# Kernel optimization log

Measured on AMD Instinct MI355X. Metric: run time of the kernel, lower is better.

The kernel has to match this reference:

```python
import jax, jax.numpy as jnp
import numpy as np

B, NW, NS, SL = 32, 500, 50, 40
EMB, HID, VOCAB, E = 300, 150, 50000, 563200
N = B * (NW + NS)
MAXPOS = 512


def _sinusoid(n_pos, d):
    pos = np.arange(n_pos)[:, None].astype(np.float64)
    i = np.arange(d)[None, :]
    ang = pos / np.power(10000.0, 2 * (i // 2) / d)
    tab = np.zeros((n_pos, d))
    tab[:, 0::2] = np.sin(ang[:, 0::2])
    tab[:, 1::2] = np.cos(ang[:, 1::2])
    tab[0] = 0.0  # padding_idx=0
    return jnp.asarray(tab, dtype=jnp.float32)

_POS_TAB = _sinusoid(MAXPOS + 1, EMB)


def setup_inputs():
    keys = iter(jax.random.split(jax.random.key(0), 48))
    def nrm(shape, s=0.05):
        return jax.random.normal(next(keys), shape, dtype=jnp.float32) * s
    inp = {}
    inp["x"] = jax.random.randint(next(keys), (B, NW), 0, VOCAB, dtype=jnp.int32)
    inp["sent_x"] = jax.random.randint(next(keys), (B, NS, SL), 0, VOCAB, dtype=jnp.int32)
    inp["edge_index"] = jax.random.randint(next(keys), (2, E), 0, N, dtype=jnp.int32)
    inp["embed_table"] = nrm((VOCAB, EMB)).at[0].set(0.0)  # padding_idx=0
    for h in range(2, 8):
        inp["conv_w%d" % h] = nrm((50, 1, h, EMB))
        inp["conv_b%d" % h] = nrm((50,))
    inp["cnn_proj_w"] = nrm((HID, EMB)); inp["cnn_proj_b"] = nrm((HID,))
    inp["lstm_w_ih_l0"] = nrm((2, 4 * HID, HID)); inp["lstm_w_hh_l0"] = nrm((2, 4 * HID, HID))
    inp["lstm_b_ih_l0"] = nrm((2, 4 * HID)); inp["lstm_b_hh_l0"] = nrm((2, 4 * HID))
    inp["lstm_w_ih_l1"] = nrm((2, 4 * HID, 2 * HID)); inp["lstm_w_hh_l1"] = nrm((2, 4 * HID, HID))
    inp["lstm_b_ih_l1"] = nrm((2, 4 * HID)); inp["lstm_b_hh_l1"] = nrm((2, 4 * HID))
    inp["lstm_proj_w"] = nrm((HID, 2 * HID)); inp["lstm_proj_b"] = nrm((HID,))
    inp["gc0_w"] = nrm((HID, EMB)); inp["gc0_b"] = nrm((HID,))
    inp["gc1_w"] = nrm((HID, HID)); inp["gc1_b"] = nrm((HID,))
    inp["gc2_w"] = nrm((HID, HID)); inp["gc2_b"] = nrm((HID,))
    return inp


def _forward(x, sent_x, edge_index, embed_table, conv_ws, conv_bs,
             cnn_proj_w, cnn_proj_b, w_ih0, w_hh0, b_ih0, b_hh0,
             w_ih1, w_hh1, b_ih1, b_hh1, lstm_proj_w, lstm_proj_b,
             gc0_w, gc0_b, gc1_w, gc1_b, gc2_w, gc2_b):
    Bsz, S, L = sent_x.shape
    Nn = Bsz * S
    emb_words = embed_table[x]                                   # [B, NW, EMB]
    tok = embed_table[sent_x].reshape(Nn, L, EMB)                # [Nn, L, EMB]
    sentlen = (sent_x != 0).sum(-1).reshape(Nn)                  # token count per sentence
    a = jnp.arange(L)
    input_pos = jnp.where(a[None, :] < sentlen[:, None], a[None, :] + 1, 0)
    enc = tok + _POS_TAB[input_pos]
    # CNN ngram features: conv heights 2..7, full-width kernels == windowed matmuls
    feats = []
    for w, b in zip(conv_ws, conv_bs):
        h = w.shape[2]
        acc = b + sum(jnp.einsum('nld,od->nlo', enc[:, k:L - h + 1 + k, :], w[:, 0, k, :]) for k in range(h))
        feats.append(jnp.max(jax.nn.relu(acc), axis=1))          # [Nn, 50]
    ngram = jnp.concatenate(feats, axis=1)                        # [Nn, 300]
    snode_pos = jnp.tile(jnp.arange(S), Bsz)
    cnn_feat = ((ngram + _POS_TAB[snode_pos]) @ cnn_proj_w.T + cnn_proj_b).reshape(Bsz, S, HID)
    glen = (sent_x[:, :, 0] != 0).sum(-1)                         # valid sentence count per graph

    def lstm_dir(xs, w_ih, w_hh, bias):
        def step(carry, xt):
            hh, cc = carry
            g = xt @ w_ih.T + hh @ w_hh.T + bias
            i, f, gg, o = jnp.split(g, 4, axis=-1)
            cc = jax.nn.sigmoid(f) * cc + jax.nn.sigmoid(i) * jnp.tanh(gg)
            hh = jax.nn.sigmoid(o) * jnp.tanh(cc)
            return (hh, cc), hh
        z = jnp.zeros((xs.shape[0], HID), xs.dtype)
        _, hs = jax.lax.scan(step, (z, z), jnp.swapaxes(xs, 0, 1))
        return jnp.swapaxes(hs, 0, 1)

    def rev_within(xs):
        # reverse only the first glen[b] steps (packed-sequence semantics)
        T = xs.shape[1]; t = jnp.arange(T)
        idx = jnp.where(t[None, :] < glen[:, None], glen[:, None] - 1 - t[None, :], t[None, :])
        return jnp.take_along_axis(xs, idx[:, :, None], axis=1)

    def bidir(xs, w_ih, w_hh, b_i, b_h):
        f = lstm_dir(xs, w_ih[0], w_hh[0], b_i[0] + b_h[0])
        r = rev_within(lstm_dir(rev_within(xs), w_ih[1], w_hh[1], b_i[1] + b_h[1]))
        return jnp.concatenate([f, r], axis=-1)

    h1 = bidir(cnn_feat, w_ih0, w_hh0, b_ih0, b_hh0)
    h2 = bidir(h1, w_ih1, w_hh1, b_ih1, b_hh1)
    mask = (jnp.arange(S)[None, :] < glen[:, None]).astype(h2.dtype)[:, :, None]
    lstm_feat = (h2 * mask) @ lstm_proj_w.T + lstm_proj_b
    sent_out = jnp.concatenate([cnn_feat, lstm_feat], axis=-1)    # [B, S, 300]
    nodes = jnp.concatenate([emb_words, sent_out], axis=1)        # [B, NW+S, 300]
    nodes = (nodes @ gc0_w.T + gc0_b).reshape(-1, HID)            # [N, 150]
    Nt = nodes.shape[0]
    loop = jnp.arange(Nt, dtype=edge_index.dtype)
    src = jnp.concatenate([edge_index[0], loop])                  # add self-loops
    dst = jnp.concatenate([edge_index[1], loop])
    deg = jax.ops.segment_sum(jnp.ones(src.shape[0], nodes.dtype), dst, num_segments=Nt)
    dis = jnp.where(deg > 0, jax.lax.rsqrt(deg), 0.0)
    norm = (dis[src] * dis[dst])[:, None]

    def gcn(xin, w, bias):
        xw = xin @ w.T
        return jax.ops.segment_sum(xw[src] * norm, dst, num_segments=Nt) + bias

    h = jax.nn.elu(gcn(nodes, gc1_w, gc1_b))
    # F.dropout with training=False -> identity
    return gcn(h, gc2_w, gc2_b), emb_words


def reference(x, sent_x, edge_index, embed_table, conv_w2, conv_b2, conv_w3, conv_b3,
              conv_w4, conv_b4, conv_w5, conv_b5, conv_w6, conv_b6, conv_w7, conv_b7,
              cnn_proj_w, cnn_proj_b, lstm_w_ih_l0, lstm_w_hh_l0, lstm_b_ih_l0, lstm_b_hh_l0,
              lstm_w_ih_l1, lstm_w_hh_l1, lstm_b_ih_l1, lstm_b_hh_l1, lstm_proj_w, lstm_proj_b,
              gc0_w, gc0_b, gc1_w, gc1_b, gc2_w, gc2_b):
    conv_ws = [conv_w2, conv_w3, conv_w4, conv_w5, conv_w6, conv_w7]
    conv_bs = [conv_b2, conv_b3, conv_b4, conv_b5, conv_b6, conv_b7]
    return _forward(x, sent_x, edge_index, embed_table, conv_ws, conv_bs,
                    cnn_proj_w, cnn_proj_b, lstm_w_ih_l0, lstm_w_hh_l0, lstm_b_ih_l0, lstm_b_hh_l0,
                    lstm_w_ih_l1, lstm_w_hh_l1, lstm_b_ih_l1, lstm_b_hh_l1, lstm_proj_w, lstm_proj_b,
                    gc0_w, gc0_b, gc1_w, gc1_b, gc2_w, gc2_b)
```

## Files before the change

kernel.cpp:

```cpp
#include <hip/hip_runtime.h>
#include <stdint.h>
#include <math.h>

#define EDGES 563200
#define NNODES 17600
#define OUT0SZ 2640000
#define MROWS 64000
#define MPAD  64016
#define KSTRIDE 2112

typedef _Float16 h2 __attribute__((ext_vector_type(2)));
typedef _Float16 h4 __attribute__((ext_vector_type(4)));
typedef _Float16 v8h __attribute__((ext_vector_type(8)));
typedef float v4f __attribute__((ext_vector_type(4)));

__device__ __forceinline__ float sigm(float x){ return 1.f / (1.f + expf(-x)); }

__device__ __forceinline__ float fdot2_(h2 a, h2 b, float c){
#if __has_builtin(__builtin_amdgcn_fdot2)
  return __builtin_amdgcn_fdot2(a, b, c, false);
#else
  return c + (float)a.x * (float)b.x + (float)a.y * (float)b.y;
#endif
}

__device__ __forceinline__ void stage16(const char* g, char* lds_base, int lane){
#if __has_builtin(__builtin_amdgcn_global_load_lds)
  __builtin_amdgcn_global_load_lds(
      (const __attribute__((address_space(1))) void*)g,
      (__attribute__((address_space(3))) void*)lds_base, 16, 0, 0);
#else
  uint4 v = *(const uint4*)g;
  *(uint4*)(lds_base + lane * 16) = v;
#endif
}

__global__ void gcnk_postab(float* __restrict__ pos){
  int idx = blockIdx.x * 256 + threadIdx.x;
  if (idx >= 513 * 300) return;
  int p = idx / 300, i = idx - p * 300;
  float v = 0.f;
  if (p != 0){
    double expo = (double)(2 * (i / 2)) / 300.0;
    double ang = (double)p / pow(10000.0, expo);
    v = (float)((i & 1) ? cos(ang) : sin(ang));
  }
  pos[idx] = v;
}

__global__ __launch_bounds__(1024)
void gcnk_prep2(const int* __restrict__ sx, int* __restrict__ sentlen,
                int* __restrict__ glen_g, int* __restrict__ rowmap){
  __shared__ int sg[32];
  int tid = threadIdx.x;
  for (int i = tid; i < 1600; i += 1024){
    int c = 0;
    for (int j = 0; j < 40; j++) c += (sx[i * 40 + j] != 0);
    sentlen[i] = c;
  }
  if (tid < 32){
    int c = 0;
    for (int s = 0; s < 50; s++) c += (sx[tid * 2000 + s * 40] != 0);
    glen_g[tid] = c; sg[tid] = c;
  }
  __syncthreads();
  for (int i = tid; i < 1600; i += 1024){
    int b = i / 50, t = i - b * 50, g = sg[b];
    rowmap[i] = b * 50 + ((t < g) ? (g - 1 - t) : t);
  }
}

__global__ void gcnk_embw(const int* __restrict__ x, const float* __restrict__ tab,
                          float4* __restrict__ out){
  int idx = blockIdx.x * 256 + threadIdx.x;
  if (idx >= 16000 * 75) return;
  int row = idx / 75, q = idx - row * 75;
  const float4* t = (const float4*)tab;
  out[idx] = t[x[row] * 75 + q];
}

__global__ void gcnk_zeroi(unsigned int* __restrict__ p, int n){
  int i = blockIdx.x * 256 + threadIdx.x;
  if (i < n) p[i] = 0u;
}

__global__ void gcnk_ench(const int* __restrict__ sx, const float* __restrict__ tab,
                          const float* __restrict__ pos, const int* __restrict__ sentlen,
                          _Float16* __restrict__ ench){
  int idx = blockIdx.x * 256 + threadIdx.x;
  if (idx >= MPAD * 75) return;
  int row = idx / 75, q = idx - row * 75;
  int d = q * 4;
  h4 o; o[0] = (_Float16)0.f; o[1] = (_Float16)0.f; o[2] = (_Float16)0.f; o[3] = (_Float16)0.f;
  if (row < MROWS){
    int n = row / 40, l = row - n * 40;
    int tok = sx[n * 40 + l];
    int p = (l < sentlen[n]) ? (l + 1) : 0;
    float4 a = *(const float4*)(tab + (size_t)tok * 300 + d);
    float4 b = *(const float4*)(pos + (size_t)p * 300 + d);
    o[0] = (_Float16)(a.x + b.x); o[1] = (_Float16)(a.y + b.y);
    o[2] = (_Float16)(a.z + b.z); o[3] = (_Float16)(a.w + b.w);
  }
  *(h4*)(ench + (size_t)row * 300 + d) = o;
}

__global__ void gcnk_bpack(const float* w2, const float* w3, const float* w4,
                           const float* w5, const float* w6, const float* w7,
                           const float* c2, const float* c3, const float* c4,
                           const float* c5, const float* c6, const float* c7,
                           _Float16* __restrict__ Bp, float* __restrict__ bias_p){
  int idx = blockIdx.x * 256 + threadIdx.x;
  if (idx < 2 * 160 * KSTRIDE){
    int n = idx / KSTRIDE, kk = idx - n * KSTRIDE;
    int g = n / 160, c = n - g * 160;
    _Float16 v = (_Float16)0.f;
    if (c < 150){
      int H = 3 * g + 2 + c / 50, o = c % 50;
      if (kk < 300 * H){
        const float* w;
        switch (H){ case 2: w = w2; break; case 3: w = w3; break;
                    case 4: w = w4; break; case 5: w = w5; break;
                    case 6: w = w6; break; default: w = w7; break; }
        v = (_Float16)w[o * 300 * H + kk];
      }
    }
    Bp[idx] = v;
  }
  if (idx < 320){
    int g = idx / 160, c = idx - g * 160;
    float bv = 0.f;
    if (c < 150){
      int H = 3 * g + 2 + c / 50, o = c % 50;
      const float* cbp;
      switch (H){ case 2: cbp = c2; break; case 3: cbp = c3; break;
                  case 4: cbp = c4; break; case 5: cbp = c5; break;
                  case 6: cbp = c6; break; default: cbp = c7; break; }
      bv = cbp[o];
    }
    bias_p[idx] = bv;
  }
}

__global__ __launch_bounds__(256)
void gcnk_convmfma(const _Float16* __restrict__ A, const _Float16* __restrict__ Bp,
                   const float* __restrict__ bias_p, unsigned int* __restrict__ ngram_u){
  __shared__ __align__(1024) char smem[36864];
  _Float16* Asm = (_Float16*)smem;
  _Float16* Bsm = (_Float16*)(smem + 16384);
  float* Cs = (float*)smem;
  const int tid = threadIdx.x;
  const int m0 = blockIdx.x * 128;
  const int grp = blockIdx.y;
  const char* Abase = (const char*)A;
  const char* Bbase = (const char*)(Bp + (size_t)grp * 160 * KSTRIDE);
  const int kmax = grp ? 2112 : 1216;
  const int w = tid >> 6, lane = tid & 63;
  const int wm = (w >> 1) * 64, wn = (w & 1) * 80;
  const int fm = lane & 15, fq = lane >> 4;
  const int lrow = lane >> 3;
  const int loff = (((lane & 7) ^ lrow) << 4);

  v4f acc[4][5] = {};

  for (int kc = 0; kc < kmax; kc += 64){
    #pragma unroll
    for (int ii = 0; ii < 4; ii++){
      int i = w * 4 + ii;
      const char* g = Abase + (size_t)(m0 + i * 8 + lrow) * 600 + kc * 2 + loff;
      stage16(g, (char*)Asm + i * 1024, lane);
    }
    #pragma unroll
    for (int jj = 0; jj < 5; jj++){
      int j = w * 5 + jj;
      const char* g = Bbase + (size_t)(j * 8 + lrow) * (KSTRIDE * 2) + kc * 2 + loff;
      stage16(g, (char*)Bsm + j * 1024, lane);
    }
    __syncthreads();
    #pragma unroll
    for (int ks = 0; ks < 2; ks++){
      const int axor = (ks * 64 + fq * 16) ^ ((fm & 7) << 4);
      v8h af[4], bf[5];
      #pragma unroll
      for (int mt = 0; mt < 4; mt++)
        af[mt] = *(const v8h*)((const char*)Asm + (wm + mt * 16 + fm) * 128 + axor);
      #pragma unroll
      for (int nt = 0; nt < 5; nt++)
        bf[nt] = *(const v8h*)((const char*)Bsm + (wn + nt * 16 + fm) * 128 + axor);
      #pragma unroll
      for (int mt = 0; mt < 4; mt++)
        #pragma unroll
        for (int nt = 0; nt < 5; nt++)
          acc[mt][nt] = __builtin_amdgcn_mfma_f32_16x16x32_f16(af[mt], bf[nt], acc[mt][nt], 0, 0, 0);
    }
    __syncthreads();
  }

  for (int p = 0; p < 5; p++){
    __syncthreads();
    #pragma unroll
    for (int nt = 0; nt < 5; nt++){
      int cstart = wn + nt * 16;
      if ((cstart >> 5) == p){
        int co = cstart - p * 32 + fm;
        #pragma unroll
        for (int mt = 0; mt < 4; mt++)
          #pragma unroll
          for (int r = 0; r < 4; r++)
            Cs[(wm + mt * 16 + fq * 4 + r) * 33 + co] = acc[mt][nt][r];
      }
    }
    __syncthreads();
    if (tid < 128){
      int cl = tid & 31, si = tid >> 5;
      int col = p * 32 + cl;
      if (col < 150){
        int H = 3 * grp + 2 + col / 50, lh = 41 - H;
        int sent = m0 / 40 + si;
        if (sent < 1600){
          int rlo = sent * 40; if (rlo < m0) rlo = m0;
          int rhi = sent * 40 + lh; if (rhi > m0 + 128) rhi = m0 + 128;
          if (rlo < rhi){
            float bv = bias_p[grp * 160 + col];
            float vmax = 0.f;
            for (int r = rlo; r < rhi; r++){
              float v = Cs[(r - m0) * 33 + cl] + bv;
              vmax = fmaxf(vmax, v);
            }
            atomicMax(ngram_u + sent * 300 + grp * 150 + col, __float_as_uint(vmax));
          }
        }
      }
    }
  }
}

template<int BM, int BN, int WMT, int WNT, int OUTH>
__global__ __launch_bounds__(256)
void gcnk_mgemm(const float* __restrict__ A, const float* __restrict__ Wt,
                const float* __restrict__ b1, const float* __restrict__ b2,
                void* __restrict__ Cv, int M, int N, int K){
  __shared__ __align__(16) _Float16 As[BM * 40];
  __shared__ __align__(16) _Float16 Bs[BN * 40];
  const int tid = threadIdx.x;
  const int m0 = blockIdx.x * BM, n0 = blockIdx.y * BN;
  const int w = tid >> 6, lane = tid & 63;
  const int wm = (w >> 1) * (WMT * 16), wn = (w & 1) * (WNT * 16);
  const int fm = lane & 15, fq = lane >> 4;
  v4f acc[WMT][WNT] = {};
  const int nch = (K + 31) >> 5;
  for (int ch = 0; ch < nch; ch++){
    int kc = ch * 32;
    #pragma unroll
    for (int j = 0; j < BM / 64; j++){
      int u = tid + 256 * j;
      int row = u >> 2, cb = (u & 3) * 8;
      int gm = m0 + row, gk = kc + cb;
      v8h vv;
      if (gm < M && gk + 8 <= K){
        const float2* p = (const float2*)(A + (size_t)gm * K + gk);
        float2 q0 = p[0], q1 = p[1], q2 = p[2], q3 = p[3];
        vv[0] = (_Float16)q0.x; vv[1] = (_Float16)q0.y;
        vv[2] = (_Float16)q1.x; vv[3] = (_Float16)q1.y;
        vv[4] = (_Float16)q2.x; vv[5] = (_Float16)q2.y;
        vv[6] = (_Float16)q3.x; vv[7] = (_Float16)q3.y;
      } else {
        #pragma unroll
        for (int e = 0; e < 8; e++)
          vv[e] = (gm < M && gk + e < K) ? (_Float16)A[(size_t)gm * K + gk + e] : (_Float16)0.f;
      }
      *(v8h*)(As + row * 40 + cb) = vv;
    }
    {
      int row = tid >> 2, cb = (tid & 3) * 8;
      int gn = n0 + row, gk = kc + cb;
      v8h vv;
      if (gn < N && gk + 8 <= K){
        const float2* p = (const float2*)(Wt + (size_t)gn * K + gk);
        float2 q0 = p[0], q1 = p[1], q2 = p[2], q3 = p[3];
        vv[0] = (_Float16)q0.x; vv[1] = (_Float16)q0.y;
        vv[2] = (_Float16)q1.x; vv[3] = (_Float16)q1.y;
        vv[4] = (_Float16)q2.x; vv[5] = (_Float16)q2.y;
        vv[6] = (_Float16)q3.x; vv[7] = (_Float16)q3.y;
      } else {
        #pragma unroll
        for (int e = 0; e < 8; e++)
          vv[e] = (gn < N && gk + e < K) ? (_Float16)Wt[(size_t)gn * K + gk + e] : (_Float16)0.f;
      }
      *(v8h*)(Bs + row * 40 + cb) = vv;
    }
    __syncthreads();
    v8h af[WMT], bf[WNT];
    #pragma unroll
    for (int mt = 0; mt < WMT; mt++)
      af[mt] = *(const v8h*)(As + (wm + mt * 16 + fm) * 40 + fq * 8);
    #pragma unroll
    for (int nt = 0; nt < WNT; nt++)
      bf[nt] = *(const v8h*)(Bs + (wn + nt * 16 + fm) * 40 + fq * 8);
    #pragma unroll
    for (int mt = 0; mt < WMT; mt++)
      #pragma unroll
      for (int nt = 0; nt < WNT; nt++)
        acc[mt][nt] = __builtin_amdgcn_mfma_f32_16x16x32_f16(af[mt], bf[nt], acc[mt][nt], 0, 0, 0);
    __syncthreads();
  }
  #pragma unroll
  for (int nt = 0; nt < WNT; nt++){
    int gn = n0 + wn + nt * 16 + fm;
    if (gn >= N) continue;
    float badd = (b1 ? b1[gn] : 0.f) + (b2 ? b2[gn] : 0.f);
    #pragma unroll
    for (int mt = 0; mt < WMT; mt++)
      #pragma unroll
      for (int r = 0; r < 4; r++){
        int gm = m0 + wm + mt * 16 + fq * 4 + r;
        if (gm < M){
          float val = acc[mt][nt][r] + badd;
          if (OUTH) ((_Float16*)Cv)[(size_t)gm * 160 + gn] = (_Float16)val;
          else      ((float*)Cv)[(size_t)gm * N + gn] = val;
        }
      }
  }
}

__global__ __launch_bounds__(256)
void gcnk_mgemmF(const float* __restrict__ A1, const int* __restrict__ mapA,
                 const float* __restrict__ A2, const int* __restrict__ mapB,
                 const int* __restrict__ glen, int usemask,
                 const float* __restrict__ apos,
                 const float* __restrict__ Wt, const float* __restrict__ b1,
                 const float* __restrict__ b2, float* __restrict__ C,
                 int M, int N, int K){
  const int BM = 64, WMT = 2, WNT = 2;
  __shared__ __align__(16) _Float16 As[BM * 40];
  __shared__ __align__(16) _Float16 Bs[64 * 40];
  const int tid = threadIdx.x;
  const int m0 = blockIdx.x * BM, n0 = blockIdx.y * 64;
  const int w = tid >> 6, lane = tid & 63;
  const int wm = (w >> 1) * (WMT * 16), wn = (w & 1) * (WNT * 16);
  const int fm = lane & 15, fq = lane >> 4;
  v4f acc[WMT][WNT] = {};
  const int nch = (K + 31) >> 5;
  for (int ch = 0; ch < nch; ch++){
    int kc = ch * 32;
    {
      int row = tid >> 2, cb = (tid & 3) * 8;
      int gm = m0 + row, gk = kc + cb;
      v8h vv;
      bool ok = (gm < M);
      if (ok && usemask){
        int b = gm / 50;
        if (gm - b * 50 >= glen[b]) ok = false;
      }
      if (!ok){
        #pragma unroll
        for (int e = 0; e < 8; e++) vv[e] = (_Float16)0.f;
      } else if (!A2){
        int r = mapA ? mapA[gm] : gm;
        const float* base = A1 + (size_t)r * K;
        if (gk + 8 <= K){
          const float2* p = (const float2*)(base + gk);
          float2 q0 = p[0], q1 = p[1], q2 = p[2], q3 = p[3];
          if (apos){
            const float2* a2 = (const float2*)(apos + (size_t)(gm % 50) * K + gk);
            float2 r0 = a2[0], r1 = a2[1], r2 = a2[2], r3 = a2[3];
            q0.x += r0.x; q0.y += r0.y; q1.x += r1.x; q1.y += r1.y;
            q2.x += r2.x; q2.y += r2.y; q3.x += r3.x; q3.y += r3.y;
          }
          vv[0] = (_Float16)q0.x; vv[1] = (_Float16)q0.y;
          vv[2] = (_Float16)q1.x; vv[3] = (_Float16)q1.y;
          vv[4] = (_Float16)q2.x; vv[5] = (_Float16)q2.y;
          vv[6] = (_Float16)q3.x; vv[7] = (_Float16)q3.y;
        } else {
          #pragma unroll
          for (int e = 0; e < 8; e++){
            int c = gk + e;
            float vf = (c < K) ? base[c] : 0.f;
            if (apos && c < K) vf += apos[(size_t)(gm % 50) * K + c];
            vv[e] = (_Float16)vf;
          }
        }
      } else {
        int rA = mapA ? mapA[gm] : gm;
        int rB = mapB ? mapB[gm] : gm;
        const float* pa = A1 + (size_t)rA * 150;
        const float* pb = A2 + (size_t)rB * 150;
        if (gk + 8 <= 150){
          const float2* p = (const float2*)(pa + gk);
          float2 q0 = p[0], q1 = p[1], q2 = p[2], q3 = p[3];
          vv[0] = (_Float16)q0.x; vv[1] = (_Float16)q0.y;
          vv[2] = (_Float16)q1.x; vv[3] = (_Float16)q1.y;
          vv[4] = (_Float16)q2.x; vv[5] = (_Float16)q2.y;
          vv[6] = (_Float16)q3.x; vv[7] = (_Float16)q3.y;
        } else if (gk >= 152 && gk + 8 <= K){
          const float2* p = (const float2*)(pb + gk - 150);
          float2 q0 = p[0], q1 = p[1], q2 = p[2], q3 = p[3];
          vv[0] = (_Float16)q0.x; vv[1] = (_Float16)q0.y;
          vv[2] = (_Float16)q1.x; vv[3] = (_Float16)q1.y;
          vv[4] = (_Float16)q2.x; vv[5] = (_Float16)q2.y;
          vv[6] = (_Float16)q3.x; vv[7] = (_Float16)q3.y;
        } else {
          #pragma unroll
          for (int e = 0; e < 8; e++){
            int c = gk + e;
            vv[e] = (c < 150) ? (_Float16)pa[c]
                  : ((c < K) ? (_Float16)pb[c - 150] : (_Float16)0.f);
          }
        }
      }
      *(v8h*)(As + row * 40 + cb) = vv;
    }
    {
      int row = tid >> 2, cb = (tid & 3) * 8;
      int gn = n0 + row, gk = kc + cb;
      v8h vv;
      if (gn < N && gk + 8 <= K){
        const float2* p = (const float2*)(Wt + (size_t)gn * K + gk);
        float2 q0 = p[0], q1 = p[1], q2 = p[2], q3 = p[3];
        vv[0] = (_Float16)q0.x; vv[1] = (_Float16)q0.y;
        vv[2] = (_Float16)q1.x; vv[3] = (_Float16)q1.y;
        vv[4] = (_Float16)q2.x; vv[5] = (_Float16)q2.y;
        vv[6] = (_Float16)q3.x; vv[7] = (_Float16)q3.y;
      } else {
        #pragma unroll
        for (int e = 0; e < 8; e++)
          vv[e] = (gn < N && gk + e < K) ? (_Float16)Wt[(size_t)gn * K + gk + e] : (_Float16)0.f;
      }
      *(v8h*)(Bs + row * 40 + cb) = vv;
    }
    __syncthreads();
    v8h af[WMT], bf[WNT];
    #pragma unroll
    for (int mt = 0; mt < WMT; mt++)
      af[mt] = *(const v8h*)(As + (wm + mt * 16 + fm) * 40 + fq * 8);
    #pragma unroll
    for (int nt = 0; nt < WNT; nt++)
      bf[nt] = *(const v8h*)(Bs + (wn + nt * 16 + fm) * 40 + fq * 8);
    #pragma unroll
    for (int mt = 0; mt < WMT; mt++)
      #pragma unroll
      for (int nt = 0; nt < WNT; nt++)
        acc[mt][nt] = __builtin_amdgcn_mfma_f32_16x16x32_f16(af[mt], bf[nt], acc[mt][nt], 0, 0, 0);
    __syncthreads();
  }
  #pragma unroll
  for (int nt = 0; nt < WNT; nt++){
    int gn = n0 + wn + nt * 16 + fm;
    if (gn >= N) continue;
    float badd = (b1 ? b1[gn] : 0.f) + (b2 ? b2[gn] : 0.f);
    #pragma unroll
    for (int mt = 0; mt < WMT; mt++)
      #pragma unroll
      for (int r = 0; r < 4; r++){
        int gm = m0 + wm + mt * 16 + fq * 4 + r;
        if (gm < M) C[(size_t)gm * N + gn] = acc[mt][nt][r] + badd;
      }
  }
}

__global__ void gcnk_nodes_in(const int* __restrict__ x, const float* __restrict__ tab,
                              const float* __restrict__ cnnf, const float* __restrict__ lstmf,
                              float* __restrict__ out){
  int idx = blockIdx.x * 256 + threadIdx.x;
  if (idx >= NNODES * 300) return;
  int nrow = idx / 300, d = idx - nrow * 300;
  int b = nrow / 550, j = nrow - b * 550;
  float v;
  if (j < 500) v = tab[x[b * 500 + j] * 300 + d];
  else {
    int r = b * 50 + (j - 500);
    v = (d < 150) ? cnnf[r * 150 + d] : lstmf[r * 150 + d - 150];
  }
  out[idx] = v;
}

__global__ void gcnk_whhpack(const float* __restrict__ whh, _Float16* __restrict__ wpad){
  int idx = blockIdx.x * 256 + threadIdx.x;
  if (idx >= 1200 * 152) return;
  int row = idx / 152, col = idx - row * 152;
  wpad[idx] = (col < 150) ? (_Float16)whh[row * 150 + col] : (_Float16)0.f;
}

__global__ __launch_bounds__(640)
void gcnk_lstm(const float* __restrict__ xf, const float* __restrict__ xr,
               const _Float16* __restrict__ wpad, float* __restrict__ fo,
               float* __restrict__ ro){
  int b = blockIdx.x >> 1, dir = blockIdx.x & 1;
  const float* xih = dir ? xr : xf;
  float* out = dir ? ro : fo;
  __shared__ __align__(16) _Float16 hh[160];
  __shared__ float gates[600];
  const int tid = threadIdx.x;

  h2 w[76];
  if (tid < 600){
    const h2* wrow = (const h2*)(wpad + ((size_t)dir * 600 + tid) * 152);
    #pragma unroll
    for (int j = 0; j < 76; j++) w[j] = wrow[j];
  }
  for (int u = tid; u < 160; u += 640) hh[u] = (_Float16)0.f;
  float creg = 0.f;
  __syncthreads();

  for (int t = 0; t < 50; t++){
    if (tid < 600){
      float acc = xih[(b * 50 + t) * 600 + tid];
      float a0 = 0.f, a1 = 0.f, a2 = 0.f, a3 = 0.f;
      #pragma unroll
      for (int j = 0; j < 19; j++){
        union { float4 f; h2 h[4]; } u;
        u.f = *(const float4*)(hh + j * 8);
        a0 = fdot2_(w[4 * j + 0], u.h[0], a0);
        a1 = fdot2_(w[4 * j + 1], u.h[1], a1);
        a2 = fdot2_(w[4 * j + 2], u.h[2], a2);
        a3 = fdot2_(w[4 * j + 3], u.h[3], a3);
      }
      gates[tid] = acc + ((a0 + a1) + (a2 + a3));
    }
    __syncthreads();
    if (tid < 150){
      float ig = sigm(gates[tid]);
      float fg = sigm(gates[150 + tid]);
      float gg = tanhf(gates[300 + tid]);
      float og = sigm(gates[450 + tid]);
      creg = fg * creg + ig * gg;
      float hn = og * tanhf(creg);
      hh[tid] = (_Float16)hn;
      out[(b * 50 + t) * 150 + tid] = hn;
    }
    __syncthreads();
  }
}

__global__ void gcnk_hist(const int* __restrict__ ei, int* __restrict__ ecnt){
  int e = blockIdx.x * 256 + threadIdx.x;
  if (e < EDGES) atomicAdd(&ecnt[ei[EDGES + e]], 1);
}

__global__ __launch_bounds__(1024)
void gcnk_scan(const int* __restrict__ ecnt, int* __restrict__ eoff,
               int* __restrict__ ecur, float* __restrict__ dis){
  __shared__ int wsum[16];
  int tid = threadIdx.x;
  int base = tid * 18;
  int pre[18];
  int s = 0;
  #pragma unroll
  for (int i = 0; i < 18; i++){
    int idx = base + i;
    int c = (idx < NNODES) ? ecnt[idx] : 0;
    if (idx < NNODES) dis[idx] = rsqrtf((float)(c + 1));
    pre[i] = s; s += c;
  }
  int lane = tid & 63, wid = tid >> 6;
  int run = s;
  #pragma unroll
  for (int off = 1; off < 64; off <<= 1){
    int y = __shfl_up(run, off, 64);
    if (lane >= off) run += y;
  }
  if (lane == 63) wsum[wid] = run;
  __syncthreads();
  if (tid == 0){
    int a = 0;
    #pragma unroll
    for (int i = 0; i < 16; i++){ int t2 = wsum[i]; wsum[i] = a; a += t2; }
  }
  __syncthreads();
  int excl = wsum[wid] + run - s;
  #pragma unroll
  for (int i = 0; i < 18; i++){
    int idx = base + i;
    if (idx < NNODES){
      int e = excl + pre[i];
      eoff[idx] = e; ecur[idx] = e;
    }
  }
}

__global__ void gcnk_scatter(const int* __restrict__ ei, int* __restrict__ ecur,
                             int* __restrict__ esrc){
  int e = blockIdx.x * 256 + threadIdx.x;
  if (e < EDGES){
    int d = ei[EDGES + e];
    int p = atomicAdd(&ecur[d], 1);
    esrc[p] = ei[e];
  }
}

__global__ __launch_bounds__(128)
void gcnk_aggcsr_h(const int* __restrict__ eoff, const int* __restrict__ ecnt,
                   const int* __restrict__ esrc, const float* __restrict__ dis,
                   const _Float16* __restrict__ xw, const float* __restrict__ bias,
                   float* __restrict__ out, int doelu){
  int d = blockIdx.x, t = threadIdx.x;
  float dd = dis[d];
  bool act = t < 75;
  float ax0 = 0.f, ay0 = 0.f, ax1 = 0.f, ay1 = 0.f;
  if (act){
    h2 v = *(const h2*)(xw + (size_t)d * 160 + 2 * t);
    ax0 = (float)v[0] * dd; ay0 = (float)v[1] * dd;
  }
  int beg = eoff[d], end = beg + ecnt[d];
  int j = beg;
  for (; j + 1 < end; j += 2){
    int s0 = esrc[j], s1 = esrc[j + 1];
    float d0 = dis[s0], d1 = dis[s1];
    if (act){
      h2 v0 = *(const h2*)(xw + (size_t)s0 * 160 + 2 * t);
      h2 v1 = *(const h2*)(xw + (size_t)s1 * 160 + 2 * t);
      ax0 += (float)v0[0] * d0; ay0 += (float)v0[1] * d0;
      ax1 += (float)v1[0] * d1; ay1 += (float)v1[1] * d1;
    }
  }
  if (j < end){
    int s = esrc[j];
    float ds_ = dis[s];
    if (act){
      h2 v = *(const h2*)(xw + (size_t)s * 160 + 2 * t);
      ax0 += (float)v[0] * ds_; ay0 += (float)v[1] * ds_;
    }
  }
  if (act){
    float o0 = (ax0 + ax1) * dd + bias[2 * t];
    float o1 = (ay0 + ay1) * dd + bias[2 * t + 1];
    if (doelu){
      o0 = (o0 > 0.f) ? o0 : expm1f(o0);
      o1 = (o1 > 0.f) ? o1 : expm1f(o1);
    }
    *(float2*)(out + (size_t)d * 150 + 2 * t) = make_float2(o0, o1);
  }
}

extern "C" void kernel_launch(void* const* d_in, const int* in_sizes, int n_in,
                              void* d_out, int out_size, void* d_ws, size_t ws_size,
                              hipStream_t stream){
  (void)in_sizes; (void)n_in; (void)out_size; (void)ws_size;

  char* wsb = (char*)d_ws;
  size_t off = 0;
  auto alloc = [&](size_t bytes) -> void* {
    void* p = wsb + off;
    off = (off + bytes + 255) & ~(size_t)255;
    return p;
  };
  float* pos_tab  = (float*)alloc(513 * 300 * 4);
  int*   sentlen  = (int*)alloc(1600 * 4);
  int*   glen     = (int*)alloc(32 * 4);
  int*   rowmap   = (int*)alloc(1600 * 4);
  float* ngram    = (float*)alloc(1600 * 300 * 4);
  float* cnn_feat = (float*)alloc(1600 * 150 * 4);
  float* xih_f    = (float*)alloc(1600 * 600 * 4);
  float* xih_r    = (float*)alloc(1600 * 600 * 4);
  float* f0       = (float*)alloc(1600 * 150 * 4);
  float* r0       = (float*)alloc(1600 * 150 * 4);
  float* f1       = (float*)alloc(1600 * 150 * 4);
  float* r1       = (float*)alloc(1600 * 150 * 4);
  float* lstm_ft  = (float*)alloc(1600 * 150 * 4);
  float* nodes_in = (float*)alloc((size_t)NNODES * 300 * 4);
  float* nodes    = (float*)alloc((size_t)NNODES * 150 * 4);
  float* dis      = (float*)alloc(NNODES * 4);
  _Float16* xwh   = (_Float16*)alloc((size_t)NNODES * 160 * 2);
  _Float16* ench  = (_Float16*)alloc((size_t)MPAD * 300 * 2);
  _Float16* Bp    = (_Float16*)alloc((size_t)2 * 160 * KSTRIDE * 2);
  float* bias_p   = (float*)alloc(320 * 4);
  _Float16* wpad0 = (_Float16*)alloc(1200 * 152 * 2);
  _Float16* wpad1 = (_Float16*)alloc(1200 * 152 * 2);
  int*   ecnt     = (int*)alloc(NNODES * 4);
  int*   eoff     = (int*)alloc(NNODES * 4);
  int*   ecur     = (int*)alloc(NNODES * 4);
  int*   esrc     = (int*)alloc(EDGES * 4);

  const int*   x   = (const int*)d_in[0];
  const int*   sx  = (const int*)d_in[1];
  const int*   ei  = (const int*)d_in[2];
  const float* tab = (const float*)d_in[3];
  const float *cw[6], *cb[6];
  for (int h = 0; h < 6; h++){ cw[h] = (const float*)d_in[4 + 2 * h]; cb[h] = (const float*)d_in[5 + 2 * h]; }
  const float* cnnw = (const float*)d_in[16]; const float* cnnb = (const float*)d_in[17];
  const float* wih0 = (const float*)d_in[18]; const float* whh0 = (const float*)d_in[19];
  const float* bih0 = (const float*)d_in[20]; const float* bhh0 = (const float*)d_in[21];
  const float* wih1 = (const float*)d_in[22]; const float* whh1 = (const float*)d_in[23];
  const float* bih1 = (const float*)d_in[24]; const float* bhh1 = (const float*)d_in[25];
  const float* lpw  = (const float*)d_in[26]; const float* lpb  = (const float*)d_in[27];
  const float* g0w  = (const float*)d_in[28]; const float* g0b  = (const float*)d_in[29];
  const float* g1w  = (const float*)d_in[30]; const float* g1b  = (const float*)d_in[31];
  const float* g2w  = (const float*)d_in[32]; const float* g2b  = (const float*)d_in[33];

  float* out0 = (float*)d_out;
  float4* out1 = (float4*)((float*)d_out + OUT0SZ);

  auto mgemmL = [&](const float* A, const float* W, const float* b1, const float* b2,
                    void* C, int M, int N, int K){
    dim3 g((M + 127) / 128, (N + 63) / 64);
    gcnk_mgemm<128, 64, 4, 2, 0><<<g, 256, 0, stream>>>(A, W, b1, b2, C, M, N, K);
  };
  auto mgemmLH = [&](const float* A, const float* W, void* C, int M, int N, int K){
    dim3 g((M + 127) / 128, (N + 63) / 64);
    gcnk_mgemm<128, 64, 4, 2, 1><<<g, 256, 0, stream>>>(A, W, nullptr, nullptr, C, M, N, K);
  };
  auto mgemmF = [&](const float* A1, const int* mapA, const float* A2, const int* mapB,
                    const int* gl, int um, const float* apos, const float* W,
                    const float* b1, const float* b2, float* C, int N, int K){
    dim3 g(25, (N + 63) / 64);
    gcnk_mgemmF<<<g, 256, 0, stream>>>(A1, mapA, A2, mapB, gl, um, apos, W, b1, b2, C, 1600, N, K);
  };

  gcnk_postab<<<602, 256, 0, stream>>>(pos_tab);
  gcnk_prep2<<<1, 1024, 0, stream>>>(sx, sentlen, glen, rowmap);
  gcnk_embw<<<4688, 256, 0, stream>>>(x, tab, out1);

  gcnk_zeroi<<<1875, 256, 0, stream>>>((unsigned int*)ngram, 1600 * 300);
  gcnk_ench<<<(MPAD * 75 + 255) / 256, 256, 0, stream>>>(sx, tab, pos_tab, sentlen, ench);
  gcnk_bpack<<<(2 * 160 * KSTRIDE + 255) / 256, 256, 0, stream>>>(
      cw[0], cw[1], cw[2], cw[3], cw[4], cw[5],
      cb[0], cb[1], cb[2], cb[3], cb[4], cb[5], Bp, bias_p);
  gcnk_whhpack<<<713, 256, 0, stream>>>(whh0, wpad0);
  gcnk_whhpack<<<713, 256, 0, stream>>>(whh1, wpad1);
  {
    dim3 g(500, 2);
    gcnk_convmfma<<<g, 256, 0, stream>>>(ench, Bp, bias_p, (unsigned int*)ngram);
  }
  mgemmF(ngram, nullptr, nullptr, nullptr, nullptr, 0, pos_tab,
         cnnw, cnnb, nullptr, cnn_feat, 150, 300);

  mgemmF(cnn_feat, nullptr, nullptr, nullptr, nullptr, 0, nullptr,
         wih0,             bih0,       bhh0,       xih_f, 600, 150);
  mgemmF(cnn_feat, rowmap,  nullptr, nullptr, nullptr, 0, nullptr,
         wih0 + 600 * 150, bih0 + 600, bhh0 + 600, xih_r, 600, 150);
  gcnk_lstm<<<64, 640, 0, stream>>>(xih_f, xih_r, wpad0, f0, r0);

  mgemmF(f0, nullptr, r0, rowmap, nullptr, 0, nullptr,
         wih1,             bih1,       bhh1,       xih_f, 600, 300);
  mgemmF(f0, rowmap, r0, nullptr, nullptr, 0, nullptr,
         wih1 + 600 * 300, bih1 + 600, bhh1 + 600, xih_r, 600, 300);
  gcnk_lstm<<<64, 640, 0, stream>>>(xih_f, xih_r, wpad1, f1, r1);

  mgemmF(f1, nullptr, r1, rowmap, glen, 1, nullptr, lpw, lpb, nullptr, lstm_ft, 150, 300);

  gcnk_nodes_in<<<20625, 256, 0, stream>>>(x, tab, cnn_feat, lstm_ft, nodes_in);
  mgemmL(nodes_in, g0w, g0b, nullptr, nodes, NNODES, 150, 300);

  gcnk_zeroi<<<69, 256, 0, stream>>>((unsigned int*)ecnt, NNODES);
  gcnk_hist<<<2200, 256, 0, stream>>>(ei, ecnt);
  gcnk_scan<<<1, 1024, 0, stream>>>(ecnt, eoff, ecur, dis);
  gcnk_scatter<<<2200, 256, 0, stream>>>(ei, ecur, esrc);

  mgemmLH(nodes, g1w, xwh, NNODES, 150, 150);
  gcnk_aggcsr_h<<<NNODES, 128, 0, stream>>>(eoff, ecnt, esrc, dis, xwh, g1b, nodes, 1);

  mgemmLH(nodes, g2w, xwh, NNODES, 150, 150);
  gcnk_aggcsr_h<<<NNODES, 128, 0, stream>>>(eoff, ecnt, esrc, dis, xwh, g2b, out0, 0);
}
```

Before: 811.0 us.

## Merge prep kernels, swizzle conv block order, and use fp16 node input for gc0 GEMM

Six small setup kernels (positional table, conv weight packing, two recurrent weight packs, two zero-fills) are merged into one launch to cut launch overhead. The conv MFMA grid is flattened and remapped so that consecutive blocks are spread across the two filter groups and row tiles. The node-input gather now writes fp16 pairs, and a new fp16-input MFMA GEMM with K fixed at 300 replaces the fp32 gc0 GEMM, halving intermediate traffic. The cost is a small precision loss on the gc0 input, plus branchy block dispatch in the merged kernel.

```diff
diff --git a/kernel.cpp b/kernel.cpp
--- a/kernel.cpp
+++ b/kernel.cpp
@@ -35,19 +35,6 @@
 #endif
 }
 
-__global__ void gcnk_postab(float* __restrict__ pos){
-  int idx = blockIdx.x * 256 + threadIdx.x;
-  if (idx >= 513 * 300) return;
-  int p = idx / 300, i = idx - p * 300;
-  float v = 0.f;
-  if (p != 0){
-    double expo = (double)(2 * (i / 2)) / 300.0;
-    double ang = (double)p / pow(10000.0, expo);
-    v = (float)((i & 1) ? cos(ang) : sin(ang));
-  }
-  pos[idx] = v;
-}
-
 __global__ __launch_bounds__(1024)
 void gcnk_prep2(const int* __restrict__ sx, int* __restrict__ sentlen,
                 int* __restrict__ glen_g, int* __restrict__ rowmap){
@@ -70,6 +57,78 @@
   }
 }
 
+__global__ __launch_bounds__(256)
+void gcnk_mergedprep(float* __restrict__ pos,
+                     const float* w2, const float* w3, const float* w4,
+                     const float* w5, const float* w6, const float* w7,
+                     const float* c2, const float* c3, const float* c4,
+                     const float* c5, const float* c6, const float* c7,
+                     _Float16* __restrict__ Bp, float* __restrict__ bias_p,
+                     const float* __restrict__ whh0, _Float16* __restrict__ wpad0,
+                     const float* __restrict__ whh1, _Float16* __restrict__ wpad1,
+                     unsigned int* __restrict__ ngram_u, unsigned int* __restrict__ ecnt_u){
+  int blk = blockIdx.x, tid = threadIdx.x;
+  if (blk < 602){
+    int idx = blk * 256 + tid;
+    if (idx >= 513 * 300) return;
+    int p = idx / 300, i = idx - p * 300;
+    float v = 0.f;
+    if (p != 0){
+      double expo = (double)(2 * (i / 2)) / 300.0;
+      double ang = (double)p / pow(10000.0, expo);
+      v = (float)((i & 1) ? cos(ang) : sin(ang));
+    }
+    pos[idx] = v;
+  } else if (blk < 3242){
+    int idx = (blk - 602) * 256 + tid;
+    if (idx < 2 * 160 * KSTRIDE){
+      int n = idx / KSTRIDE, kk = idx - n * KSTRIDE;
+      int g = n / 160, c = n - g * 160;
+      _Float16 v = (_Float16)0.f;
+      if (c < 150){
+        int H = 3 * g + 2 + c / 50, o = c % 50;
+        if (kk < 300 * H){
+          const float* w;
+          switch (H){ case 2: w = w2; break; case 3: w = w3; break;
+                      case 4: w = w4; break; case 5: w = w5; break;
+                      case 6: w = w6; break; default: w = w7; break; }
+          v = (_Float16)w[o * 300 * H + kk];
+        }
+      }
+      Bp[idx] = v;
+    }
+    if (idx < 320){
+      int g = idx / 160, c = idx - g * 160;
+      float bv = 0.f;
+      if (c < 150){
+        int H = 3 * g + 2 + c / 50, o = c % 50;
+        const float* cbp;
+        switch (H){ case 2: cbp = c2; break; case 3: cbp = c3; break;
+                    case 4: cbp = c4; break; case 5: cbp = c5; break;
+                    case 6: cbp = c6; break; default: cbp = c7; break; }
+        bv = cbp[o];
+      }
+      bias_p[idx] = bv;
+    }
+  } else if (blk < 3955){
+    int idx = (blk - 3242) * 256 + tid;
+    if (idx >= 1200 * 152) return;
+    int row = idx / 152, col = idx - row * 152;
+    wpad0[idx] = (col < 150) ? (_Float16)whh0[row * 150 + col] : (_Float16)0.f;
+  } else if (blk < 4668){
+    int idx = (blk - 3955) * 256 + tid;
+    if (idx >= 1200 * 152) return;
+    int row = idx / 152, col = idx - row * 152;
+    wpad1[idx] = (col < 150) ? (_Float16)whh1[row * 150 + col] : (_Float16)0.f;
+  } else if (blk < 6543){
+    int idx = (blk - 4668) * 256 + tid;
+    if (idx < 1600 * 300) ngram_u[idx] = 0u;
+  } else {
+    int idx = (blk - 6543) * 256 + tid;
+    if (idx < NNODES) ecnt_u[idx] = 0u;
+  }
+}
+
 __global__ void gcnk_embw(const int* __restrict__ x, const float* __restrict__ tab,
                           float4* __restrict__ out){
   int idx = blockIdx.x * 256 + threadIdx.x;
@@ -77,11 +136,6 @@
   int row = idx / 75, q = idx - row * 75;
   const float4* t = (const float4*)tab;
   out[idx] = t[x[row] * 75 + q];
-}
-
-__global__ void gcnk_zeroi(unsigned int* __restrict__ p, int n){
-  int i = blockIdx.x * 256 + threadIdx.x;
-  if (i < n) p[i] = 0u;
 }
 
 __global__ void gcnk_ench(const int* __restrict__ sx, const float* __restrict__ tab,
@@ -104,43 +158,6 @@
   *(h4*)(ench + (size_t)row * 300 + d) = o;
 }
 
-__global__ void gcnk_bpack(const float* w2, const float* w3, const float* w4,
-                           const float* w5, const float* w6, const float* w7,
-                           const float* c2, const float* c3, const float* c4,
-                           const float* c5, const float* c6, const float* c7,
-                           _Float16* __restrict__ Bp, float* __restrict__ bias_p){
-  int idx = blockIdx.x * 256 + threadIdx.x;
-  if (idx < 2 * 160 * KSTRIDE){
-    int n = idx / KSTRIDE, kk = idx - n * KSTRIDE;
-    int g = n / 160, c = n - g * 160;
-    _Float16 v = (_Float16)0.f;
-    if (c < 150){
-      int H = 3 * g + 2 + c / 50, o = c % 50;
-      if (kk < 300 * H){
-        const float* w;
-        switch (H){ case 2: w = w2; break; case 3: w = w3; break;
-                    case 4: w = w4; break; case 5: w = w5; break;
-                    case 6: w = w6; break; default: w = w7; break; }
-        v = (_Float16)w[o * 300 * H + kk];
-      }
-    }
-    Bp[idx] = v;
-  }
-  if (idx < 320){
-    int g = idx / 160, c = idx - g * 160;
-    float bv = 0.f;
-    if (c < 150){
-      int H = 3 * g + 2 + c / 50, o = c % 50;
-      const float* cbp;
-      switch (H){ case 2: cbp = c2; break; case 3: cbp = c3; break;
-                  case 4: cbp = c4; break; case 5: cbp = c5; break;
-                  case 6: cbp = c6; break; default: cbp = c7; break; }
-      bv = cbp[o];
-    }
-    bias_p[idx] = bv;
-  }
-}
-
 __global__ __launch_bounds__(256)
 void gcnk_convmfma(const _Float16* __restrict__ A, const _Float16* __restrict__ Bp,
                    const float* __restrict__ bias_p, unsigned int* __restrict__ ngram_u){
@@ -149,8 +166,10 @@
   _Float16* Bsm = (_Float16*)(smem + 16384);
   float* Cs = (float*)smem;
   const int tid = threadIdx.x;
-  const int m0 = blockIdx.x * 128;
-  const int grp = blockIdx.y;
+  const int bid = blockIdx.x;
+  const int work = (bid & 7) * 125 + (bid >> 3);
+  const int m0 = (work >> 1) * 128;
+  const int grp = work & 1;
   const char* Abase = (const char*)A;
   const char* Bbase = (const char*)(Bp + (size_t)grp * 160 * KSTRIDE);
   const int kmax = grp ? 2112 : 1216;
@@ -318,6 +337,86 @@
           if (OUTH) ((_Float16*)Cv)[(size_t)gm * 160 + gn] = (_Float16)val;
           else      ((float*)Cv)[(size_t)gm * N + gn] = val;
         }
+      }
+  }
+}
+
+__global__ __launch_bounds__(256)
+void gcnk_mgemmH(const _Float16* __restrict__ Ah, const float* __restrict__ Wt,
+                 const float* __restrict__ b1, float* __restrict__ C, int M, int N){
+  const int K = 300;
+  __shared__ __align__(16) _Float16 As[128 * 40];
+  __shared__ __align__(16) _Float16 Bs[64 * 40];
+  const int tid = threadIdx.x;
+  const int m0 = blockIdx.x * 128, n0 = blockIdx.y * 64;
+  const int w = tid >> 6, lane = tid & 63;
+  const int wm = (w >> 1) * 64, wn = (w & 1) * 32;
+  const int fm = lane & 15, fq = lane >> 4;
+  v4f acc[4][2] = {};
+  for (int ch = 0; ch < 10; ch++){
+    int kc = ch * 32;
+    #pragma unroll
+    for (int j = 0; j < 2; j++){
+      int u = tid + 256 * j;
+      int row = u >> 2, cb = (u & 3) * 8;
+      int gm = m0 + row, gk = kc + cb;
+      v8h vv;
+      if (gm < M && gk + 8 <= K){
+        const char* p = (const char*)(Ah + (size_t)gm * 300 + gk);
+        union { uint2 u2[2]; v8h v; } t;
+        t.u2[0] = *(const uint2*)p; t.u2[1] = *(const uint2*)(p + 8);
+        vv = t.v;
+      } else {
+        #pragma unroll
+        for (int e = 0; e < 8; e++)
+          vv[e] = (gm < M && gk + e < K) ? Ah[(size_t)gm * 300 + gk + e] : (_Float16)0.f;
+      }
+      *(v8h*)(As + row * 40 + cb) = vv;
+    }
+    {
+      int row = tid >> 2, cb = (tid & 3) * 8;
+      int gn = n0 + row, gk = kc + cb;
+      v8h vv;
+      if (gn < N && gk + 8 <= K){
+        const float2* p = (const float2*)(Wt + (size_t)gn * K + gk);
+        float2 q0 = p[0], q1 = p[1], q2 = p[2], q3 = p[3];
+        vv[0] = (_Float16)q0.x; vv[1] = (_Float16)q0.y;
+        vv[2] = (_Float16)q1.x; vv[3] = (_Float16)q1.y;
+        vv[4] = (_Float16)q2.x; vv[5] = (_Float16)q2.y;
+        vv[6] = (_Float16)q3.x; vv[7] = (_Float16)q3.y;
+      } else {
+        #pragma unroll
+        for (int e = 0; e < 8; e++)
+          vv[e] = (gn < N && gk + e < K) ? (_Float16)Wt[(size_t)gn * K + gk + e] : (_Float16)0.f;
+      }
+      *(v8h*)(Bs + row * 40 + cb) = vv;
+    }
+    __syncthreads();
+    v8h af[4], bf[2];
+    #pragma unroll
+    for (int mt = 0; mt < 4; mt++)
+      af[mt] = *(const v8h*)(As + (wm + mt * 16 + fm) * 40 + fq * 8);
+    #pragma unroll
+    for (int nt = 0; nt < 2; nt++)
+      bf[nt] = *(const v8h*)(Bs + (wn + nt * 16 + fm) * 40 + fq * 8);
+    #pragma unroll
+    for (int mt = 0; mt < 4; mt++)
+      #pragma unroll
+      for (int nt = 0; nt < 2; nt++)
+        acc[mt][nt] = __builtin_amdgcn_mfma_f32_16x16x32_f16(af[mt], bf[nt], acc[mt][nt], 0, 0, 0);
+    __syncthreads();
+  }
+  #pragma unroll
+  for (int nt = 0; nt < 2; nt++){
+    int gn = n0 + wn + nt * 16 + fm;
+    if (gn >= N) continue;
+    float badd = b1[gn];
+    #pragma unroll
+    for (int mt = 0; mt < 4; mt++)
+      #pragma unroll
+      for (int r = 0; r < 4; r++){
+        int gm = m0 + wm + mt * 16 + fq * 4 + r;
+        if (gm < M) C[(size_t)gm * N + gn] = acc[mt][nt][r] + badd;
       }
   }
 }
@@ -457,27 +556,23 @@
   }
 }
 
-__global__ void gcnk_nodes_in(const int* __restrict__ x, const float* __restrict__ tab,
-                              const float* __restrict__ cnnf, const float* __restrict__ lstmf,
-                              float* __restrict__ out){
+__global__ void gcnk_nodes_in_h(const int* __restrict__ x, const float* __restrict__ tab,
+                                const float* __restrict__ cnnf, const float* __restrict__ lstmf,
+                                h2* __restrict__ out){
   int idx = blockIdx.x * 256 + threadIdx.x;
-  if (idx >= NNODES * 300) return;
-  int nrow = idx / 300, d = idx - nrow * 300;
+  if (idx >= NNODES * 150) return;
+  int nrow = idx / 150, q = idx - nrow * 150;
+  int d = q * 2;
   int b = nrow / 550, j = nrow - b * 550;
-  float v;
-  if (j < 500) v = tab[x[b * 500 + j] * 300 + d];
+  float2 v;
+  if (j < 500) v = *(const float2*)(tab + (size_t)x[b * 500 + j] * 300 + d);
   else {
     int r = b * 50 + (j - 500);
-    v = (d < 150) ? cnnf[r * 150 + d] : lstmf[r * 150 + d - 150];
-  }
-  out[idx] = v;
-}
-
-__global__ void gcnk_whhpack(const float* __restrict__ whh, _Float16* __restrict__ wpad){
-  int idx = blockIdx.x * 256 + threadIdx.x;
-  if (idx >= 1200 * 152) return;
-  int row = idx / 152, col = idx - row * 152;
-  wpad[idx] = (col < 150) ? (_Float16)whh[row * 150 + col] : (_Float16)0.f;
+    if (d < 150) v = *(const float2*)(cnnf + (size_t)r * 150 + d);
+    else         v = *(const float2*)(lstmf + (size_t)r * 150 + d - 150);
+  }
+  h2 o; o[0] = (_Float16)v.x; o[1] = (_Float16)v.y;
+  out[idx] = o;
 }
 
 __global__ __launch_bounds__(640)
@@ -656,7 +751,7 @@
   float* f1       = (float*)alloc(1600 * 150 * 4);
   float* r1       = (float*)alloc(1600 * 150 * 4);
   float* lstm_ft  = (float*)alloc(1600 * 150 * 4);
-  float* nodes_in = (float*)alloc((size_t)NNODES * 300 * 4);
+  h2*    nodes_ih = (h2*)alloc((size_t)NNODES * 150 * 4);
   float* nodes    = (float*)alloc((size_t)NNODES * 150 * 4);
   float* dis      = (float*)alloc(NNODES * 4);
   _Float16* xwh   = (_Float16*)alloc((size_t)NNODES * 160 * 2);
@@ -689,11 +784,6 @@
   float* out0 = (float*)d_out;
   float4* out1 = (float4*)((float*)d_out + OUT0SZ);
 
-  auto mgemmL = [&](const float* A, const float* W, const float* b1, const float* b2,
-                    void* C, int M, int N, int K){
-    dim3 g((M + 127) / 128, (N + 63) / 64);
-    gcnk_mgemm<128, 64, 4, 2, 0><<<g, 256, 0, stream>>>(A, W, b1, b2, C, M, N, K);
-  };
   auto mgemmLH = [&](const float* A, const float* W, void* C, int M, int N, int K){
     dim3 g((M + 127) / 128, (N + 63) / 64);
     gcnk_mgemm<128, 64, 4, 2, 1><<<g, 256, 0, stream>>>(A, W, nullptr, nullptr, C, M, N, K);
@@ -705,21 +795,16 @@
     gcnk_mgemmF<<<g, 256, 0, stream>>>(A1, mapA, A2, mapB, gl, um, apos, W, b1, b2, C, 1600, N, K);
   };
 
-  gcnk_postab<<<602, 256, 0, stream>>>(pos_tab);
   gcnk_prep2<<<1, 1024, 0, stream>>>(sx, sentlen, glen, rowmap);
+  gcnk_mergedprep<<<6612, 256, 0, stream>>>(
+      pos_tab, cw[0], cw[1], cw[2], cw[3], cw[4], cw[5],
+      cb[0], cb[1], cb[2], cb[3], cb[4], cb[5], Bp, bias_p,
+      whh0, wpad0, whh1, wpad1, (unsigned int*)ngram, (unsigned int*)ecnt);
   gcnk_embw<<<4688, 256, 0, stream>>>(x, tab, out1);
-
-  gcnk_zeroi<<<1875, 256, 0, stream>>>((unsigned int*)ngram, 1600 * 300);
   gcnk_ench<<<(MPAD * 75 + 255) / 256, 256, 0, stream>>>(sx, tab, pos_tab, sentlen, ench);
-  gcnk_bpack<<<(2 * 160 * KSTRIDE + 255) / 256, 256, 0, stream>>>(
-      cw[0], cw[1], cw[2], cw[3], cw[4], cw[5],
-      cb[0], cb[1], cb[2], cb[3], cb[4], cb[5], Bp, bias_p);
-  gcnk_whhpack<<<713, 256, 0, stream>>>(whh0, wpad0);
-  gcnk_whhpack<<<713, 256, 0, stream>>>(whh1, wpad1);
-  {
-    dim3 g(500, 2);
-    gcnk_convmfma<<<g, 256, 0, stream>>>(ench, Bp, bias_p, (unsigned int*)ngram);
-  }
+
+  gcnk_convmfma<<<1000, 256, 0, stream>>>(ench, Bp, bias_p, (unsigned int*)ngram);
+
   mgemmF(ngram, nullptr, nullptr, nullptr, nullptr, 0, pos_tab,
          cnnw, cnnb, nullptr, cnn_feat, 150, 300);
 
@@ -737,10 +822,12 @@
 
   mgemmF(f1, nullptr, r1, rowmap, glen, 1, nullptr, lpw, lpb, nullptr, lstm_ft, 150, 300);
 
-  gcnk_nodes_in<<<20625, 256, 0, stream>>>(x, tab, cnn_feat, lstm_ft, nodes_in);
-  mgemmL(nodes_in, g0w, g0b, nullptr, nodes, NNODES, 150, 300);
-
-  gcnk_zeroi<<<69, 256, 0, stream>>>((unsigned int*)ecnt, NNODES);
+  gcnk_nodes_in_h<<<(NNODES * 150 + 255) / 256, 256, 0, stream>>>(x, tab, cnn_feat, lstm_ft, nodes_ih);
+  {
+    dim3 g(138, 3);
+    gcnk_mgemmH<<<g, 256, 0, stream>>>((const _Float16*)nodes_ih, g0w, g0b, nodes, NNODES, 150);
+  }
+
   gcnk_hist<<<2200, 256, 0, stream>>>(ei, ecnt);
   gcnk_scan<<<1, 1024, 0, stream>>>(ecnt, eoff, ecur, dis);
   gcnk_scatter<<<2200, 256, 0, stream>>>(ei, ecur, esrc);
```

Measured after the change: 800.3 us. About the same (-1.3%).
